# Performance work log

Measured on AMD Instinct MI355X. Metric: run time of the kernel, lower is better.

Reference implementation:

```python
import jax, jax.numpy as jnp
import numpy as np

N_NODES = 50000
N_EDGES = 800000
D_FEAT = 64          # per-node feature dim
HIDDEN = 128         # fc1 output dim; fc1 input = 2*D_FEAT


def setup_inputs() -> dict:
    key = jax.random.key(0)
    k1, k2, k3 = jax.random.split(key, 3)
    x = jax.random.normal(k1, (N_NODES, D_FEAT), dtype=jnp.float32)
    edge_index = jax.random.randint(k2, (2, N_EDGES), 0, N_NODES, dtype=jnp.int64)
    # fc1: Linear(2*D_FEAT, HIDDEN); torch Linear weight is [out, in]
    W = jax.random.normal(k3, (HIDDEN, 2 * D_FEAT), dtype=jnp.float32) * (1.0 / np.sqrt(2 * D_FEAT))
    b = jnp.zeros((HIDDEN,), dtype=jnp.float32)
    return {"x": x, "edge_index": edge_index, "W": W, "b": b}


def reference(x, edge_index, W, b):
    # Gather source-node features along edges, sum-scatter to destinations.
    src, dst = edge_index[0], edge_index[1]
    gathered = x[src]  # [E, D_FEAT] -- dominant memory traffic
    neigh = jax.ops.segment_sum(gathered, dst, num_segments=x.shape[0])  # [N, D_FEAT]
    # Concat self features with aggregated neighbor features, then Linear+ReLU.
    h = jnp.concatenate([x, neigh], axis=-1)          # [N, 2*D_FEAT]
    out = jax.nn.relu(h @ W.T + b)                    # [N, HIDDEN]
    return out
```

## Files before the change

kernel.cpp:

```cpp
#include <hip/hip_runtime.h>

#define N_NODES 50000
#define N_EDGES 800000
#define DFEAT 64
#define HID 128
#define NBKT 782
#define NSEG 391
#define SEGW 16
#define CAP_S 1536
#define NSTR 66

#define XB2 1563
#define WB2 8
#define EB2 391

typedef __bf16 bf16x8 __attribute__((ext_vector_type(8)));
typedef float f32x4 __attribute__((ext_vector_type(4)));

__device__ inline unsigned short f2bf(float f) {
  unsigned u = __float_as_uint(f);
  return (unsigned short)((u + 0x7FFFu + ((u >> 16) & 1u)) >> 16);
}
__device__ inline float bf2f(unsigned short h) {
  return __uint_as_float(((unsigned)h) << 16);
}

__global__ __launch_bounds__(512) void k_prep(const float* __restrict__ x,
                                              const float* __restrict__ W,
                                              const int* __restrict__ ei,
                                              unsigned short* __restrict__ xb,
                                              unsigned short* __restrict__ Wb,
                                              unsigned int* __restrict__ coarse) {
  int bid = blockIdx.x;
  const int tid = threadIdx.x;
  if (bid < XB2) {
    int t = bid * 512 + tid;
    if (t < N_NODES * DFEAT / 4) {
      float4 v = *(const float4*)&x[t * 4];
      ushort4 o = {f2bf(v.x), f2bf(v.y), f2bf(v.z), f2bf(v.w)};
      *(ushort4*)&xb[t * 4] = o;
    }
    return;
  }
  bid -= XB2;
  if (bid < WB2) {
    int t = bid * 512 + tid;
    float4 v = *(const float4*)&W[t * 4];
    ushort4 o = {f2bf(v.x), f2bf(v.y), f2bf(v.z), f2bf(v.w)};
    *(ushort4*)&Wb[t * 4] = o;
    return;
  }
  bid -= WB2;
  __shared__ int lcnt[NBKT];
  for (int i = tid; i < NBKT; i += 512) lcnt[i] = 0;
  __syncthreads();

  int e0 = (bid * 512 + tid) * 4;
  if (e0 < N_EDGES) {
    int4 s4 = *(const int4*)&ei[e0];
    int4 d4 = *(const int4*)&ei[N_EDGES + e0];
    int ss[4] = {s4.x, s4.y, s4.z, s4.w};
    int dd[4] = {d4.x, d4.y, d4.z, d4.w};
#pragma unroll
    for (int i = 0; i < 4; ++i) {
      int bkt = dd[i] >> 6;
      int rank = atomicAdd(&lcnt[bkt], 1);
      if (rank < SEGW - 1)
        coarse[(size_t)bkt * (NSEG * SEGW) + bid * SEGW + 1 + rank] =
            ((unsigned)dd[i] << 16) | (unsigned)ss[i];
    }
  }
  __syncthreads();
  for (int i = tid; i < NBKT; i += 512) {
    int c = lcnt[i];
    coarse[(size_t)i * (NSEG * SEGW) + bid * SEGW] =
        (unsigned)(c < SEGW - 1 ? c : SEGW - 1);
  }
}

__global__ __launch_bounds__(512) void k_gnn(const unsigned short* __restrict__ xb,
                                             const unsigned short* __restrict__ Wb,
                                             const unsigned int* __restrict__ coarse,
                                             const float* __restrict__ bv,
                                             float* __restrict__ out) {
  __shared__ unsigned int q[CAP_S];
  __shared__ unsigned int sq[CAP_S];
  __shared__ unsigned int ns_u[32 * NSTR];
  __shared__ int scnt[NSEG];
  __shared__ int lcnt[64];
  __shared__ int lbase[65];
  __shared__ int qn;

  const int tid = threadIdx.x;
  const int b = blockIdx.x;
  const int nb = b * 64;
  const unsigned int* base = coarse + (size_t)b * (NSEG * SEGW);

  if (tid < 64) lcnt[tid] = 0;
  if (tid == 0) qn = 0;
  for (int i = tid; i < NSEG; i += 512) {
    int c = (int)base[i * SEGW];
    scnt[i] = c < SEGW - 1 ? c : SEGW - 1;
  }
  __syncthreads();

  const int NU4 = NSEG * SEGW / 4;
  for (int i = tid; i < NU4; i += 512) {
    uint4 w = ((const uint4*)base)[i];
    int seg = i >> 2;
    int wi = (i & 3) * 4;
    int cw = scnt[seg];
    unsigned e[4] = {w.x, w.y, w.z, w.w};
#pragma unroll
    for (int k = 0; k < 4; ++k) {
      int widx = wi + k;
      if (widx >= 1 && widx <= cw) {
        int pos = atomicAdd(&qn, 1);
        if (pos < CAP_S) q[pos] = e[k] & 0x003fffffu;
      }
    }
  }
  __syncthreads();

  int cnt = qn < CAP_S ? qn : CAP_S;

  int myrank[3], myidx[3], nloc = 0;
  for (int i = tid; i < cnt; i += 512) {
    int rel = (int)(q[i] >> 16);
    myrank[nloc] = atomicAdd(&lcnt[rel], 1);
    myidx[nloc] = i;
    ++nloc;
  }
  __syncthreads();
  if (tid < 64) {
    int v = lcnt[tid];
    int inc = v;
#pragma unroll
    for (int o = 1; o < 64; o <<= 1) {
      int u = __shfl_up(inc, o);
      if (tid >= o) inc += u;
    }
    lbase[tid] = inc - v;
    if (tid == 63) lbase[64] = inc;
  }
  __syncthreads();
  for (int k = 0; k < nloc; ++k) {
    unsigned e = q[myidx[k]];
    sq[lbase[e >> 16] + myrank[k]] = e;
  }
  __syncthreads();

  const int wave = tid >> 6;
  const int lane = tid & 63;
  const int eslot = lane >> 4;
  const int c = lane & 15;
  const uint2* xu2 = (const uint2*)xb;

#pragma unroll
  for (int i2 = 0; i2 < 8; ++i2) {
    int n = wave * 8 + i2;
    int beg = lbase[n], end = lbase[n + 1];
    float f0 = 0.f, f1 = 0.f, f2 = 0.f, f3 = 0.f;
    float g0 = 0.f, g1 = 0.f, g2 = 0.f, g3 = 0.f;
    int j = beg + eslot;
    for (; j + 4 < end; j += 8) {
      unsigned e0 = sq[j], e1 = sq[j + 4];
      uint2 v0 = xu2[(e0 & 0xffffu) * 16 + c];
      uint2 v1 = xu2[(e1 & 0xffffu) * 16 + c];
      f0 += bf2f((unsigned short)(v0.x & 0xffffu)); f1 += bf2f((unsigned short)(v0.x >> 16));
      f2 += bf2f((unsigned short)(v0.y & 0xffffu)); f3 += bf2f((unsigned short)(v0.y >> 16));
      g0 += bf2f((unsigned short)(v1.x & 0xffffu)); g1 += bf2f((unsigned short)(v1.x >> 16));
      g2 += bf2f((unsigned short)(v1.y & 0xffffu)); g3 += bf2f((unsigned short)(v1.y >> 16));
    }
    for (; j < end; j += 4) {
      unsigned e = sq[j];
      uint2 v = xu2[(e & 0xffffu) * 16 + c];
      f0 += bf2f((unsigned short)(v.x & 0xffffu)); f1 += bf2f((unsigned short)(v.x >> 16));
      f2 += bf2f((unsigned short)(v.y & 0xffffu)); f3 += bf2f((unsigned short)(v.y >> 16));
    }
    f0 += g0; f1 += g1; f2 += g2; f3 += g3;
    f0 += __shfl_xor(f0, 16); f0 += __shfl_xor(f0, 32);
    f1 += __shfl_xor(f1, 16); f1 += __shfl_xor(f1, 32);
    f2 += __shfl_xor(f2, 16); f2 += __shfl_xor(f2, 32);
    f3 += __shfl_xor(f3, 16); f3 += __shfl_xor(f3, 32);
    if (eslot == 0) {
      ns_u[(2 * c) * NSTR + n] = (unsigned)f2bf(f0) | ((unsigned)f2bf(f1) << 16);
      ns_u[(2 * c + 1) * NSTR + n] = (unsigned)f2bf(f2) | ((unsigned)f2bf(f3) << 16);
    }
  }
  __syncthreads();

  const int g = wave & 3;
  const int o = wave >> 2;
  const int l15 = lane & 15;
  const int quad = lane >> 4;
  const int node0 = nb + g * 16;

  int anode = node0 + l15;
  if (anode >= N_NODES) anode = N_NODES - 1;
  const unsigned short* hx = xb + (size_t)anode * DFEAT;

  bf16x8 fa0 = *(const bf16x8*)(hx + quad * 8);
  bf16x8 fa1 = *(const bf16x8*)(hx + 32 + quad * 8);
  bf16x8 fa2, fa3;
  {
    int m = g * 16 + l15;
    union { unsigned u[4]; bf16x8 v; } c2, c3;
#pragma unroll
    for (int i = 0; i < 4; ++i) {
      c2.u[i] = ns_u[(quad * 4 + i) * NSTR + m];
      c3.u[i] = ns_u[(16 + quad * 4 + i) * NSTR + m];
    }
    fa2 = c2.v;
    fa3 = c3.v;
  }

  f32x4 accr[4];
#pragma unroll
  for (int t = 0; t < 4; ++t) accr[t] = (f32x4){0.f, 0.f, 0.f, 0.f};

#pragma unroll
  for (int t = 0; t < 4; ++t) {
    int nt = o * 4 + t;
    const unsigned short* wr = Wb + (size_t)(nt * 16 + l15) * (2 * DFEAT) + quad * 8;
    bf16x8 b0 = *(const bf16x8*)(wr);
    bf16x8 b1 = *(const bf16x8*)(wr + 32);
    bf16x8 b2 = *(const bf16x8*)(wr + 64);
    bf16x8 b3 = *(const bf16x8*)(wr + 96);
    accr[t] = __builtin_amdgcn_mfma_f32_16x16x32_bf16(fa0, b0, accr[t], 0, 0, 0);
    accr[t] = __builtin_amdgcn_mfma_f32_16x16x32_bf16(fa1, b1, accr[t], 0, 0, 0);
    accr[t] = __builtin_amdgcn_mfma_f32_16x16x32_bf16(fa2, b2, accr[t], 0, 0, 0);
    accr[t] = __builtin_amdgcn_mfma_f32_16x16x32_bf16(fa3, b3, accr[t], 0, 0, 0);
  }

#pragma unroll
  for (int t = 0; t < 4; ++t) {
    int nt = o * 4 + t;
    float bias = bv[nt * 16 + l15];
#pragma unroll
    for (int r = 0; r < 4; ++r) {
      int node = node0 + quad * 4 + r;
      if (node < N_NODES) {
        float v = accr[t][r] + bias;
        out[(size_t)node * HID + nt * 16 + l15] = v > 0.f ? v : 0.f;
      }
    }
  }
}

extern "C" void kernel_launch(void* const* d_in, const int* in_sizes, int n_in,
                              void* d_out, int out_size, void* d_ws, size_t ws_size,
                              hipStream_t stream) {
  const float* x = (const float*)d_in[0];
  const int* ei = (const int*)d_in[1];
  const float* W = (const float*)d_in[2];
  const float* b = (const float*)d_in[3];
  float* out = (float*)d_out;

  char* ws = (char*)d_ws;
  unsigned int* coarse = (unsigned int*)ws;   ws += (size_t)NBKT * NSEG * SEGW * 4;
  unsigned short* xb   = (unsigned short*)ws; ws += (size_t)N_NODES * DFEAT * 2;
  unsigned short* Wb   = (unsigned short*)ws; ws += (size_t)HID * 2 * DFEAT * 2;

  k_prep<<<XB2 + WB2 + EB2, 512, 0, stream>>>(x, W, ei, xb, Wb, coarse);
  k_gnn<<<NBKT, 512, 0, stream>>>(xb, Wb, coarse, b, out);
}
```

Baseline: 125.3 us.

## Replace segmented coarse buckets with global atomic-reserved compact bucket buffers

The edge bucketing no longer writes fixed 16-slot segments per prep block, which k_gnn had to read in full and compact through an extra shared queue. Each prep block now reserves a contiguous range in a per-bucket global buffer with one global atomicAdd per bucket and writes its entries compactly. k_gnn then reads only the valid entries, which cuts read traffic and removes a compaction pass. The neighbor gather loop is also unrolled to four independent loads per iteration for more memory-level parallelism; the cost is a memsetAsync for the counters, global atomics, and nondeterministic edge order within a bucket.

```diff
diff --git a/kernel.cpp b/kernel.cpp
--- a/kernel.cpp
+++ b/kernel.cpp
@@ -5,9 +5,7 @@
 #define DFEAT 64
 #define HID 128
 #define NBKT 782
-#define NSEG 391
-#define SEGW 16
-#define CAP_S 1536
+#define CAP_B 1280
 #define NSTR 66
 
 #define XB2 1563
@@ -30,7 +28,8 @@
                                               const int* __restrict__ ei,
                                               unsigned short* __restrict__ xb,
                                               unsigned short* __restrict__ Wb,
-                                              unsigned int* __restrict__ coarse) {
+                                              unsigned int* __restrict__ gbuf,
+                                              int* __restrict__ bcnt) {
   int bid = blockIdx.x;
   const int tid = threadIdx.x;
   if (bid < XB2) {
@@ -52,83 +51,70 @@
   }
   bid -= WB2;
   __shared__ int lcnt[NBKT];
+  __shared__ int lbase[NBKT];
   for (int i = tid; i < NBKT; i += 512) lcnt[i] = 0;
   __syncthreads();
 
   int e0 = (bid * 512 + tid) * 4;
-  if (e0 < N_EDGES) {
+  unsigned ent[4];
+  int bkt[4], rnk[4];
+  const bool act = e0 < N_EDGES;
+  if (act) {
     int4 s4 = *(const int4*)&ei[e0];
     int4 d4 = *(const int4*)&ei[N_EDGES + e0];
     int ss[4] = {s4.x, s4.y, s4.z, s4.w};
     int dd[4] = {d4.x, d4.y, d4.z, d4.w};
 #pragma unroll
     for (int i = 0; i < 4; ++i) {
-      int bkt = dd[i] >> 6;
-      int rank = atomicAdd(&lcnt[bkt], 1);
-      if (rank < SEGW - 1)
-        coarse[(size_t)bkt * (NSEG * SEGW) + bid * SEGW + 1 + rank] =
-            ((unsigned)dd[i] << 16) | (unsigned)ss[i];
+      bkt[i] = dd[i] >> 6;
+      ent[i] = ((unsigned)(dd[i] & 63) << 16) | (unsigned)ss[i];
+      rnk[i] = atomicAdd(&lcnt[bkt[i]], 1);
     }
   }
   __syncthreads();
   for (int i = tid; i < NBKT; i += 512) {
     int c = lcnt[i];
-    coarse[(size_t)i * (NSEG * SEGW) + bid * SEGW] =
-        (unsigned)(c < SEGW - 1 ? c : SEGW - 1);
+    lbase[i] = c ? atomicAdd(&bcnt[i], c) : 0;
+  }
+  __syncthreads();
+  if (act) {
+#pragma unroll
+    for (int i = 0; i < 4; ++i) {
+      int slot = lbase[bkt[i]] + rnk[i];
+      if (slot < CAP_B)
+        gbuf[(size_t)bkt[i] * CAP_B + slot] = ent[i];
+    }
   }
 }
 
 __global__ __launch_bounds__(512) void k_gnn(const unsigned short* __restrict__ xb,
                                              const unsigned short* __restrict__ Wb,
-                                             const unsigned int* __restrict__ coarse,
+                                             const unsigned int* __restrict__ gbuf,
+                                             const int* __restrict__ bcnt,
                                              const float* __restrict__ bv,
                                              float* __restrict__ out) {
-  __shared__ unsigned int q[CAP_S];
-  __shared__ unsigned int sq[CAP_S];
+  __shared__ unsigned int sq[CAP_B];
   __shared__ unsigned int ns_u[32 * NSTR];
-  __shared__ int scnt[NSEG];
   __shared__ int lcnt[64];
   __shared__ int lbase[65];
-  __shared__ int qn;
 
   const int tid = threadIdx.x;
   const int b = blockIdx.x;
   const int nb = b * 64;
-  const unsigned int* base = coarse + (size_t)b * (NSEG * SEGW);
 
   if (tid < 64) lcnt[tid] = 0;
-  if (tid == 0) qn = 0;
-  for (int i = tid; i < NSEG; i += 512) {
-    int c = (int)base[i * SEGW];
-    scnt[i] = c < SEGW - 1 ? c : SEGW - 1;
-  }
-  __syncthreads();
-
-  const int NU4 = NSEG * SEGW / 4;
-  for (int i = tid; i < NU4; i += 512) {
-    uint4 w = ((const uint4*)base)[i];
-    int seg = i >> 2;
-    int wi = (i & 3) * 4;
-    int cw = scnt[seg];
-    unsigned e[4] = {w.x, w.y, w.z, w.w};
-#pragma unroll
-    for (int k = 0; k < 4; ++k) {
-      int widx = wi + k;
-      if (widx >= 1 && widx <= cw) {
-        int pos = atomicAdd(&qn, 1);
-        if (pos < CAP_S) q[pos] = e[k] & 0x003fffffu;
-      }
-    }
-  }
-  __syncthreads();
-
-  int cnt = qn < CAP_S ? qn : CAP_S;
-
-  int myrank[3], myidx[3], nloc = 0;
+  __syncthreads();
+
+  int cnt = bcnt[b];
+  if (cnt > CAP_B) cnt = CAP_B;
+  const unsigned int* g = gbuf + (size_t)b * CAP_B;
+
+  unsigned ent[3];
+  int rnk[3], nloc = 0;
   for (int i = tid; i < cnt; i += 512) {
-    int rel = (int)(q[i] >> 16);
-    myrank[nloc] = atomicAdd(&lcnt[rel], 1);
-    myidx[nloc] = i;
+    unsigned e = g[i];
+    ent[nloc] = e;
+    rnk[nloc] = atomicAdd(&lcnt[e >> 16], 1);
     ++nloc;
   }
   __syncthreads();
@@ -144,10 +130,8 @@
     if (tid == 63) lbase[64] = inc;
   }
   __syncthreads();
-  for (int k = 0; k < nloc; ++k) {
-    unsigned e = q[myidx[k]];
-    sq[lbase[e >> 16] + myrank[k]] = e;
-  }
+  for (int k = 0; k < nloc; ++k)
+    sq[lbase[ent[k] >> 16] + rnk[k]] = ent[k];
   __syncthreads();
 
   const int wave = tid >> 6;
@@ -162,15 +146,23 @@
     int beg = lbase[n], end = lbase[n + 1];
     float f0 = 0.f, f1 = 0.f, f2 = 0.f, f3 = 0.f;
     float g0 = 0.f, g1 = 0.f, g2 = 0.f, g3 = 0.f;
+    float h0 = 0.f, h1 = 0.f, h2 = 0.f, h3 = 0.f;
+    float p0 = 0.f, p1 = 0.f, p2 = 0.f, p3 = 0.f;
     int j = beg + eslot;
-    for (; j + 4 < end; j += 8) {
-      unsigned e0 = sq[j], e1 = sq[j + 4];
+    for (; j + 12 < end; j += 16) {
+      unsigned e0 = sq[j], e1 = sq[j + 4], e2 = sq[j + 8], e3 = sq[j + 12];
       uint2 v0 = xu2[(e0 & 0xffffu) * 16 + c];
       uint2 v1 = xu2[(e1 & 0xffffu) * 16 + c];
+      uint2 v2 = xu2[(e2 & 0xffffu) * 16 + c];
+      uint2 v3 = xu2[(e3 & 0xffffu) * 16 + c];
       f0 += bf2f((unsigned short)(v0.x & 0xffffu)); f1 += bf2f((unsigned short)(v0.x >> 16));
       f2 += bf2f((unsigned short)(v0.y & 0xffffu)); f3 += bf2f((unsigned short)(v0.y >> 16));
       g0 += bf2f((unsigned short)(v1.x & 0xffffu)); g1 += bf2f((unsigned short)(v1.x >> 16));
       g2 += bf2f((unsigned short)(v1.y & 0xffffu)); g3 += bf2f((unsigned short)(v1.y >> 16));
+      h0 += bf2f((unsigned short)(v2.x & 0xffffu)); h1 += bf2f((unsigned short)(v2.x >> 16));
+      h2 += bf2f((unsigned short)(v2.y & 0xffffu)); h3 += bf2f((unsigned short)(v2.y >> 16));
+      p0 += bf2f((unsigned short)(v3.x & 0xffffu)); p1 += bf2f((unsigned short)(v3.x >> 16));
+      p2 += bf2f((unsigned short)(v3.y & 0xffffu)); p3 += bf2f((unsigned short)(v3.y >> 16));
     }
     for (; j < end; j += 4) {
       unsigned e = sq[j];
@@ -178,7 +170,8 @@
       f0 += bf2f((unsigned short)(v.x & 0xffffu)); f1 += bf2f((unsigned short)(v.x >> 16));
       f2 += bf2f((unsigned short)(v.y & 0xffffu)); f3 += bf2f((unsigned short)(v.y >> 16));
     }
-    f0 += g0; f1 += g1; f2 += g2; f3 += g3;
+    f0 += g0 + h0 + p0; f1 += g1 + h1 + p1;
+    f2 += g2 + h2 + p2; f3 += g3 + h3 + p3;
     f0 += __shfl_xor(f0, 16); f0 += __shfl_xor(f0, 32);
     f1 += __shfl_xor(f1, 16); f1 += __shfl_xor(f1, 32);
     f2 += __shfl_xor(f2, 16); f2 += __shfl_xor(f2, 32);
@@ -190,11 +183,11 @@
   }
   __syncthreads();
 
-  const int g = wave & 3;
+  const int g2 = wave & 3;
   const int o = wave >> 2;
   const int l15 = lane & 15;
   const int quad = lane >> 4;
-  const int node0 = nb + g * 16;
+  const int node0 = nb + g2 * 16;
 
   int anode = node0 + l15;
   if (anode >= N_NODES) anode = N_NODES - 1;
@@ -204,7 +197,7 @@
   bf16x8 fa1 = *(const bf16x8*)(hx + 32 + quad * 8);
   bf16x8 fa2, fa3;
   {
-    int m = g * 16 + l15;
+    int m = g2 * 16 + l15;
     union { unsigned u[4]; bf16x8 v; } c2, c3;
 #pragma unroll
     for (int i = 0; i < 4; ++i) {
@@ -258,10 +251,12 @@
   float* out = (float*)d_out;
 
   char* ws = (char*)d_ws;
-  unsigned int* coarse = (unsigned int*)ws;   ws += (size_t)NBKT * NSEG * SEGW * 4;
-  unsigned short* xb   = (unsigned short*)ws; ws += (size_t)N_NODES * DFEAT * 2;
-  unsigned short* Wb   = (unsigned short*)ws; ws += (size_t)HID * 2 * DFEAT * 2;
-
-  k_prep<<<XB2 + WB2 + EB2, 512, 0, stream>>>(x, W, ei, xb, Wb, coarse);
-  k_gnn<<<NBKT, 512, 0, stream>>>(xb, Wb, coarse, b, out);
-}
+  unsigned int* gbuf = (unsigned int*)ws;     ws += (size_t)NBKT * CAP_B * 4;
+  unsigned short* xb = (unsigned short*)ws;   ws += (size_t)N_NODES * DFEAT * 2;
+  unsigned short* Wb = (unsigned short*)ws;   ws += (size_t)HID * 2 * DFEAT * 2;
+  int* bcnt = (int*)ws;                       ws += (size_t)NBKT * 4 + 192;
+
+  hipMemsetAsync(bcnt, 0, NBKT * sizeof(int), stream);
+  k_prep<<<XB2 + WB2 + EB2, 512, 0, stream>>>(x, W, ei, xb, Wb, gbuf, bcnt);
+  k_gnn<<<NBKT, 512, 0, stream>>>(xb, Wb, gbuf, bcnt, b, out);
+}
```

Result: slower. 131.0 us (+4.5%).
